# Kernel optimization log

Measured on AMD Instinct MI355X. Metric: run time of the kernel, lower is better.

The kernel has to match this reference:

```python
import jax, jax.numpy as jnp
import numpy as np

B, T, D_MODEL, N_HEAD = 2, 2048, 1024, 16
HEAD_DIM = D_MODEL // N_HEAD
CHUNK, POLY = 16, 1
SCALE = HEAD_DIM ** -0.5


def alpert_basis(L):
    # poly_order=1: constant + linear Legendre-like columns, L2-normalized per column
    t = jnp.linspace(-1.0, 1.0, L)
    W = jnp.stack([jnp.ones_like(t), t], axis=1)  # [L, 2]
    return W / jnp.linalg.norm(W, axis=0, keepdims=True)


def setup_inputs() -> dict:
    key = jax.random.key(0)
    ks = jax.random.split(key, 10)
    d = D_MODEL
    nrm = lambda k, shape, s=0.02: (jax.random.normal(k, shape, jnp.float32) * s)
    return {
        'x': jax.random.normal(ks[0], (B, T, d), jnp.float32),
        'Wq': nrm(ks[1], (d, d)),
        'Wk': nrm(ks[2], (d, d)),
        'Wv': nrm(ks[3], (d, d)),
        'Wo': nrm(ks[4], (d, d)),
        'gate_w': nrm(ks[5], (d, d)),
        'gate_b': jnp.zeros((d,), jnp.float32),
        'A': nrm(ks[6], (N_HEAD, HEAD_DIM, HEAD_DIM)),
        'jump_scale': jnp.ones((1,), jnp.float32),
        'jump_bias': jnp.zeros((1,), jnp.float32),
        'sink_scalar': nrm(ks[7], (1, N_HEAD, 1, 1)),
        'v_null': nrm(ks[8], (1, N_HEAD, 1, HEAD_DIM)),
    }


def _forward(x, Wq, Wk, Wv, Wo, gate_w, gate_b, A, jump_scale, jump_bias, sink_scalar, v_null):
    Bx, Tx, C = x.shape
    H, Dh = N_HEAD, HEAD_DIM
    NEG = jnp.float32(-1e30)

    def lin(W):  # torch Linear: y = x @ W.T, W is [out, in]
        y = jnp.einsum('btc,dc->btd', x, W)
        return y.reshape(Bx, Tx, H, Dh).transpose(0, 2, 1, 3)  # [B,H,T,Dh]

    q_raw, k_raw, v_val = lin(Wq), lin(Wk), lin(Wv)
    g = jax.nn.sigmoid(jnp.einsum('btc,dc->btd', x, gate_w) + gate_b)
    gate = g.reshape(Bx, Tx, H, Dh).transpose(0, 2, 1, 3)

    # symmetric mean/std normalization (torch std is unbiased -> ddof=1)
    ms = 0.5 * (q_raw.mean(-1, keepdims=True) + k_raw.mean(-1, keepdims=True))
    ss = 0.5 * (jnp.std(q_raw, -1, keepdims=True, ddof=1) + jnp.std(k_raw, -1, keepdims=True, ddof=1))
    q_norm = (q_raw - ms) / (ss + 1e-6)
    k_norm = (k_raw - ms) / (ss + 1e-6)

    # RoPE (half-split variant as in source)
    inv = 1.0 / (10000.0 ** (jnp.arange(0, Dh, 2, dtype=jnp.float32) / Dh))
    fr = jnp.arange(Tx, dtype=jnp.float32)[:, None] * inv[None, :]  # [T, Dh/2]
    cos, sin = jnp.cos(fr)[None, None], jnp.sin(fr)[None, None]

    def rope(z):
        z1, z2 = z[..., 0::2], z[..., 1::2]
        return jnp.concatenate([-z2 * sin + z1 * cos, z1 * sin + z2 * cos], axis=-1)

    S = A - jnp.swapaxes(A, -1, -2)  # skew-symmetric per head
    wedge = lambda z: z + jnp.einsum('bhtd,hde->bhte', z, S)
    q_geo, k_geo = wedge(rope(q_norm)), wedge(rope(k_norm))

    W_b = alpert_basis(CHUNK)  # [L, K]
    N, K, L = Tx // CHUNK, W_b.shape[1], CHUNK
    to_chunks = lambda z: z.reshape(Bx, H, N, L, Dh).transpose(2, 0, 1, 3, 4)  # [N,B,H,L,Dh]
    qx, kx, gx = to_chunks(q_geo), to_chunks(k_geo), to_chunks(gate)

    hist0 = jnp.zeros((Bx, H, N, K, Dh), jnp.float32)
    last0 = jnp.zeros((Bx, H, 1, Dh), jnp.float32)
    idx = jnp.arange(N)

    def step(carry, xs):
        hist, last, i = carry
        q_c, k_c, g_c = xs  # [B,H,L,Dh]
        k_coef = jnp.einsum('bhld,lk->bhkd', k_c, W_b)
        sc = jnp.einsum('bhkd,bhnkd->bhn', k_coef, hist) * SCALE
        sc = jnp.where(idx < i, sc, NEG)  # mask unfilled history slots
        w = jax.nn.softmax(sc, axis=-1)
        retr = jnp.einsum('bhn,bhnkd->bhkd', w, hist)
        q_rec = jnp.einsum('bhkd,lk->bhld', retr, W_b)
        jg = jax.nn.sigmoid(sc.max(-1)[..., None, None] * jump_scale + jump_bias)  # [B,H,1,1]
        inj = jnp.where(i > 0, (1.0 - jg) * last + jg * q_rec, 0.0)
        q_out = jnp.cumsum(g_c * q_c, axis=2) + inj
        hist = hist.at[:, :, i].set(jnp.einsum('bhld,lk->bhkd', q_out, W_b))
        return (hist, q_out[:, :, -1:, :], i + 1), q_out

    _, q_outs = jax.lax.scan(step, (hist0, last0, jnp.int32(0)), (qx, kx, gx))
    Q = q_outs.transpose(1, 2, 0, 3, 4).reshape(Bx, H, Tx, Dh)

    att = jnp.einsum('bhtd,bhsd->bhts', Q, k_geo) * SCALE
    causal = jnp.tril(jnp.ones((Tx, Tx), bool))
    att = jnp.where(causal, att, NEG)
    null = jnp.broadcast_to(sink_scalar, (Bx, H, Tx, 1))
    probs = jax.nn.softmax(jnp.concatenate([att, null], axis=-1), axis=-1)
    out = jnp.einsum('bhts,bhsd->bhtd', probs[..., :Tx], v_val) + probs[..., Tx:] * v_null
    out = out.transpose(0, 2, 1, 3).reshape(Bx, Tx, C)
    return jnp.einsum('btc,dc->btd', out, Wo)


def reference(x, Wq, Wk, Wv, Wo, gate_w, gate_b, A, jump_scale, jump_bias, sink_scalar, v_null):
    return _forward(x, Wq, Wk, Wv, Wo, gate_w, gate_b, A, jump_scale, jump_bias, sink_scalar, v_null)
```

## Files before the change

kernel.cpp:

```cpp
#include <hip/hip_runtime.h>
#include <math.h>

#define NB 2
#define NT 2048
#define NH 16
#define DH 64
#define DM 1024

using bf8   = __attribute__((ext_vector_type(8))) short;
using f32x4 = __attribute__((ext_vector_type(4))) float;

static __device__ __forceinline__ ushort f2bf(float f) {
    union { float f; unsigned u; } c; c.f = f;
    unsigned u = c.u + 0x7FFFu + ((c.u >> 16) & 1u);
    return (ushort)(u >> 16);
}
static __device__ __forceinline__ float bf2f(ushort u) {
    union { unsigned u; float f; } c; c.u = ((unsigned)u) << 16;
    return c.f;
}

static __device__ __forceinline__ float wbf(int l, int k) {
    if (k == 0) return 0.25f;
    const float invn = 1.0f / sqrtf(1360.0f / 225.0f);
    return (-1.0f + (2.0f / 15.0f) * (float)l) * invn;
}

__global__ __launch_bounds__(256) void cast3_kernel(
    const float* __restrict__ x, const float* __restrict__ wv,
    const float* __restrict__ wo, ushort* __restrict__ xb, ushort* __restrict__ wb)
{
    const int id = blockIdx.x * 256 + threadIdx.x;
    const int XQ = (NB * NT * DM) / 4;
    const int WQ = (DM * DM) / 4;
    const float4* src;
    ushort* dst;
    if (id < XQ) {
        src = (const float4*)x + id;
        dst = xb + (size_t)id * 4;
    } else {
        const int r = id - XQ;
        const int wi = r / WQ, off = r % WQ;
        const float* w = (wi == 0) ? wv : wo;
        src = (const float4*)w + off;
        dst = wb + (size_t)wi * DM * DM + (size_t)off * 4;
    }
    const float4 v = *src;
    ushort4 o;
    o.x = f2bf(v.x); o.y = f2bf(v.y); o.z = f2bf(v.z); o.w = f2bf(v.w);
    *(ushort4*)dst = o;
}

__global__ __launch_bounds__(256) void gemm3m_kernel(
    const float* __restrict__ x, const float* __restrict__ Wq,
    const float* __restrict__ Wk, const float* __restrict__ gw,
    const float* __restrict__ gbias,
    float* __restrict__ oq, float* __restrict__ ok, float* __restrict__ og)
{
    __shared__ ushort Ah[128][40], Am[128][40], Al[128][40];
    __shared__ ushort Bh[64][40],  Bm[64][40],  Bl[64][40];
    const int z = blockIdx.z;
    const float* Bw = (z == 0) ? Wq : (z == 1) ? Wk : gw;
    float* C = (z == 0) ? oq : (z == 1) ? ok : og;
    const int tid = threadIdx.x;
    const int l = tid & 63, w = tid >> 6;
    const int wr = w >> 1, wc = w & 1;
    const int lr = l & 15, g = l >> 4;
    const int row0 = blockIdx.y * 128, col0 = blockIdx.x * 64;
    f32x4 acc[4][2];
    #pragma unroll
    for (int mi = 0; mi < 4; ++mi)
        #pragma unroll
        for (int ni = 0; ni < 2; ++ni) acc[mi][ni] = (f32x4){0.f, 0.f, 0.f, 0.f};
    const int sa_row = tid >> 1, sa_col = (tid & 1) * 16;
    const int sb_row = tid >> 2, sb_col = (tid & 3) * 8;
    const float* Ap = x  + (size_t)(row0 + sa_row) * DM + sa_col;
    const float* Bp = Bw + (size_t)(col0 + sb_row) * DM + sb_col;
    for (int k0 = 0; k0 < DM; k0 += 32) {
        float av[16], bv[8];
        *(float4*)&av[0]  = *(const float4*)(Ap + k0);
        *(float4*)&av[4]  = *(const float4*)(Ap + k0 + 4);
        *(float4*)&av[8]  = *(const float4*)(Ap + k0 + 8);
        *(float4*)&av[12] = *(const float4*)(Ap + k0 + 12);
        *(float4*)&bv[0]  = *(const float4*)(Bp + k0);
        *(float4*)&bv[4]  = *(const float4*)(Bp + k0 + 4);
        __syncthreads();
        #pragma unroll
        for (int c = 0; c < 16; c += 4) {
            ushort4 hh, mm, ll;
            ushort* hp = (ushort*)&hh;
            ushort* mp = (ushort*)&mm;
            ushort* lp = (ushort*)&ll;
            #pragma unroll
            for (int u = 0; u < 4; ++u) {
                const float v = av[c + u];
                const ushort hu = f2bf(v);
                const float r1 = v - bf2f(hu);
                const ushort mu = f2bf(r1);
                const ushort lu = f2bf(r1 - bf2f(mu));
                hp[u] = hu; mp[u] = mu; lp[u] = lu;
            }
            *(ushort4*)&Ah[sa_row][sa_col + c] = hh;
            *(ushort4*)&Am[sa_row][sa_col + c] = mm;
            *(ushort4*)&Al[sa_row][sa_col + c] = ll;
        }
        #pragma unroll
        for (int c = 0; c < 8; c += 4) {
            ushort4 hh, mm, ll;
            ushort* hp = (ushort*)&hh;
            ushort* mp = (ushort*)&mm;
            ushort* lp = (ushort*)&ll;
            #pragma unroll
            for (int u = 0; u < 4; ++u) {
                const float v = bv[c + u];
                const ushort hu = f2bf(v);
                const float r1 = v - bf2f(hu);
                const ushort mu = f2bf(r1);
                const ushort lu = f2bf(r1 - bf2f(mu));
                hp[u] = hu; mp[u] = mu; lp[u] = lu;
            }
            *(ushort4*)&Bh[sb_row][sb_col + c] = hh;
            *(ushort4*)&Bm[sb_row][sb_col + c] = mm;
            *(ushort4*)&Bl[sb_row][sb_col + c] = ll;
        }
        __syncthreads();
        bf8 ah[4], am[4], al[4], bh[2], bm[2], bl[2];
        #pragma unroll
        for (int mi = 0; mi < 4; ++mi) {
            ah[mi] = *(const bf8*)&Ah[wr * 64 + mi * 16 + lr][g * 8];
            am[mi] = *(const bf8*)&Am[wr * 64 + mi * 16 + lr][g * 8];
            al[mi] = *(const bf8*)&Al[wr * 64 + mi * 16 + lr][g * 8];
        }
        #pragma unroll
        for (int ni = 0; ni < 2; ++ni) {
            bh[ni] = *(const bf8*)&Bh[wc * 32 + ni * 16 + lr][g * 8];
            bm[ni] = *(const bf8*)&Bm[wc * 32 + ni * 16 + lr][g * 8];
            bl[ni] = *(const bf8*)&Bl[wc * 32 + ni * 16 + lr][g * 8];
        }
        #pragma unroll
        for (int mi = 0; mi < 4; ++mi)
            #pragma unroll
            for (int ni = 0; ni < 2; ++ni) {
                acc[mi][ni] = __builtin_amdgcn_mfma_f32_16x16x32_bf16(ah[mi], bh[ni], acc[mi][ni], 0, 0, 0);
                acc[mi][ni] = __builtin_amdgcn_mfma_f32_16x16x32_bf16(ah[mi], bm[ni], acc[mi][ni], 0, 0, 0);
                acc[mi][ni] = __builtin_amdgcn_mfma_f32_16x16x32_bf16(am[mi], bh[ni], acc[mi][ni], 0, 0, 0);
                acc[mi][ni] = __builtin_amdgcn_mfma_f32_16x16x32_bf16(am[mi], bm[ni], acc[mi][ni], 0, 0, 0);
                acc[mi][ni] = __builtin_amdgcn_mfma_f32_16x16x32_bf16(ah[mi], bl[ni], acc[mi][ni], 0, 0, 0);
                acc[mi][ni] = __builtin_amdgcn_mfma_f32_16x16x32_bf16(al[mi], bh[ni], acc[mi][ni], 0, 0, 0);
            }
    }
    #pragma unroll
    for (int mi = 0; mi < 4; ++mi) {
        const int m0 = row0 + wr * 64 + mi * 16 + g * 4;
        const int bb = m0 >> 11, t0 = m0 & 2047;
        #pragma unroll
        for (int ni = 0; ni < 2; ++ni) {
            const int n = col0 + wc * 32 + ni * 16 + lr;
            const int h = n >> 6, dh = n & 63;
            #pragma unroll
            for (int r = 0; r < 4; ++r) {
                float v = acc[mi][ni][r];
                if (z == 2) v = 1.0f / (1.0f + __expf(-(v + gbias[n])));
                C[(((size_t)(bb * NH + h)) * NT + (t0 + r)) * DH + dh] = v;
            }
        }
    }
}

__global__ __launch_bounds__(256) void gemm_bf16_kernel(
    const ushort* __restrict__ Ab, const ushort* __restrict__ Bb,
    float* __restrict__ Cp)
{
    __shared__ ushort Al[128][40];
    __shared__ ushort Bl[64][40];
    const int tid = threadIdx.x;
    const int l = tid & 63, w = tid >> 6;
    const int wr = w >> 1, wc = w & 1;
    const int lr = l & 15, g = l >> 4;
    const int row0 = blockIdx.y * 128, col0 = blockIdx.x * 64;
    f32x4 acc[4][2];
    #pragma unroll
    for (int mi = 0; mi < 4; ++mi)
        #pragma unroll
        for (int ni = 0; ni < 2; ++ni) acc[mi][ni] = (f32x4){0.f, 0.f, 0.f, 0.f};
    const int sa_row = tid >> 1, sa_half = (tid & 1) * 16;
    const int sb_row = tid >> 2, sb_q = (tid & 3) * 8;
    const ushort* Ap = Ab + (size_t)(row0 + sa_row) * DM + sa_half;
    const ushort* Bp = Bb + (size_t)(col0 + sb_row) * DM + sb_q;
    for (int k0 = 0; k0 < DM; k0 += 32) {
        const uint4 a0 = *(const uint4*)(Ap + k0);
        const uint4 a1 = *(const uint4*)(Ap + k0 + 8);
        const uint4 b0 = *(const uint4*)(Bp + k0);
        __syncthreads();
        *(uint4*)&Al[sa_row][sa_half]     = a0;
        *(uint4*)&Al[sa_row][sa_half + 8] = a1;
        *(uint4*)&Bl[sb_row][sb_q]        = b0;
        __syncthreads();
        bf8 a[4], b[2];
        #pragma unroll
        for (int mi = 0; mi < 4; ++mi) a[mi] = *(const bf8*)&Al[wr * 64 + mi * 16 + lr][g * 8];
        #pragma unroll
        for (int ni = 0; ni < 2; ++ni) b[ni] = *(const bf8*)&Bl[wc * 32 + ni * 16 + lr][g * 8];
        #pragma unroll
        for (int mi = 0; mi < 4; ++mi)
            #pragma unroll
            for (int ni = 0; ni < 2; ++ni)
                acc[mi][ni] = __builtin_amdgcn_mfma_f32_16x16x32_bf16(a[mi], b[ni], acc[mi][ni], 0, 0, 0);
    }
    #pragma unroll
    for (int mi = 0; mi < 4; ++mi) {
        const int m0 = row0 + wr * 64 + mi * 16 + g * 4;
        #pragma unroll
        for (int ni = 0; ni < 2; ++ni) {
            const int n = col0 + wc * 32 + ni * 16 + lr;
            #pragma unroll
            for (int r = 0; r < 4; ++r)
                Cp[(size_t)(m0 + r) * DM + n] = acc[mi][ni][r];
        }
    }
}

__global__ __launch_bounds__(256) void nrw_kernel(
    const float* __restrict__ qraw, const float* __restrict__ kraw,
    const float* __restrict__ Amat, float* __restrict__ gateq,
    ushort* __restrict__ kgb,
    float* __restrict__ kcoefA, float* __restrict__ R0A,
    float* __restrict__ R1A, float* __restrict__ r15A)
{
    __shared__ float S[64][64];
    __shared__ float zq[4][64];
    __shared__ float zk[4][64];
    const int bh = blockIdx.x;
    const int h = bh & (NH - 1);
    const int tid = threadIdx.x;
    const int g = tid >> 6, lane = tid & 63;
    for (int idx = tid; idx < 4096; idx += 256) {
        const int d = idx >> 6, e = idx & 63;
        S[d][e] = Amat[(size_t)h * 4096 + d * 64 + e] - Amat[(size_t)h * 4096 + e * 64 + d];
    }
    __syncthreads();
    const int j = lane & 31;
    const float invf = powf(10000.0f, -(float)(2 * j) * (1.0f / 64.0f));
    const int t0 = blockIdx.y * 64 + g * 16;
    float kc0 = 0.f, kc1 = 0.f, run = 0.f, Ra0 = 0.f, Ra1 = 0.f;
    for (int r = 0; r < 16; ++r) {
        const int t = t0 + r;
        const size_t base = ((size_t)bh * NT + t) * DH;
        const float qv = qraw[base + lane];
        const float kv = kraw[base + lane];
        float sq = qv, sk = kv, qq = qv * qv, kk2 = kv * kv;
        #pragma unroll
        for (int off = 32; off; off >>= 1) {
            sq += __shfl_xor(sq, off);
            sk += __shfl_xor(sk, off);
            qq += __shfl_xor(qq, off);
            kk2 += __shfl_xor(kk2, off);
        }
        const float mq = sq * (1.0f / 64.0f), mk = sk * (1.0f / 64.0f);
        const float vq = (qq - 64.0f * mq * mq) * (1.0f / 63.0f);
        const float vk = (kk2 - 64.0f * mk * mk) * (1.0f / 63.0f);
        const float ms = 0.5f * (mq + mk);
        const float ss = 0.5f * (sqrtf(fmaxf(vq, 0.0f)) + sqrtf(fmaxf(vk, 0.0f)));
        const float rinv = 1.0f / (ss + 1e-6f);
        const float qn = (qv - ms) * rinv;
        const float kn = (kv - ms) * rinv;
        const float q1 = __shfl(qn, 2 * j), q2 = __shfl(qn, 2 * j + 1);
        const float k1 = __shfl(kn, 2 * j), k2 = __shfl(kn, 2 * j + 1);
        float sn, cs;
        sincosf((float)t * invf, &sn, &cs);
        const float rq = (lane < 32) ? (q1 * cs - q2 * sn) : (q1 * sn + q2 * cs);
        const float rk = (lane < 32) ? (k1 * cs - k2 * sn) : (k1 * sn + k2 * cs);
        zq[g][lane] = rq;
        zk[g][lane] = rk;
        float aq = 0.0f, ak = 0.0f;
        #pragma unroll 8
        for (int d = 0; d < 64; ++d) {
            const float sde = S[d][lane];
            aq = fmaf(zq[g][d], sde, aq);
            ak = fmaf(zk[g][d], sde, ak);
        }
        const float qgv = rq + aq;
        const float kgv = rk + ak;
        const float gv = gateq[base + lane];
        const float qgpv = gv * qgv;
        gateq[base + lane] = qgpv;
        kgb[base + lane] = f2bf(kgv);
        kc0 = fmaf(kgv, 0.25f, kc0);
        kc1 = fmaf(kgv, wbf(r, 1), kc1);
        run += qgpv;
        Ra0 = fmaf(run, 0.25f, Ra0);
        Ra1 = fmaf(run, wbf(r, 1), Ra1);
    }
    const int unit = bh * 128 + blockIdx.y * 4 + g;
    kcoefA[(size_t)unit * 128 + lane] = kc0;
    kcoefA[(size_t)unit * 128 + 64 + lane] = kc1;
    R0A[(size_t)unit * 64 + lane] = Ra0;
    R1A[(size_t)unit * 64 + lane] = Ra1;
    r15A[(size_t)unit * 64 + lane] = run;
}

__global__ __launch_bounds__(256) void scan_vgemm_kernel(
    const float* __restrict__ kcoefA, const float* __restrict__ R0A,
    const float* __restrict__ R1A, const float* __restrict__ r15A,
    const float* __restrict__ jscale, const float* __restrict__ jbias,
    float* __restrict__ r0O, float* __restrict__ r1O,
    float* __restrict__ lpO, float* __restrict__ jgO,
    const ushort* __restrict__ xb, const ushort* __restrict__ Wb,
    ushort* __restrict__ Vt)
{
    __shared__ char smem[100864];
    if (blockIdx.x >= 32) {
        const int gi = blockIdx.x - 32;
        const int col0 = (gi & 15) * 64;
        const int row0 = (gi >> 4) * 128;
        ushort (*Al)[40] = (ushort(*)[40])smem;
        ushort (*Bl)[40] = (ushort(*)[40])(smem + 10240);
        const int tid = threadIdx.x;
        const int l = tid & 63, w = tid >> 6;
        const int wr = w >> 1, wc = w & 1;
        const int lr = l & 15, g = l >> 4;
        f32x4 acc[4][2];
        #pragma unroll
        for (int mi = 0; mi < 4; ++mi)
            #pragma unroll
            for (int ni = 0; ni < 2; ++ni) acc[mi][ni] = (f32x4){0.f, 0.f, 0.f, 0.f};
        const int sa_row = tid >> 1, sa_half = (tid & 1) * 16;
        const int sb_row = tid >> 2, sb_q = (tid & 3) * 8;
        const ushort* Ap = xb + (size_t)(row0 + sa_row) * DM + sa_half;
        const ushort* Bp = Wb + (size_t)(col0 + sb_row) * DM + sb_q;
        for (int k0 = 0; k0 < DM; k0 += 32) {
            const uint4 a0 = *(const uint4*)(Ap + k0);
            const uint4 a1 = *(const uint4*)(Ap + k0 + 8);
            const uint4 b0 = *(const uint4*)(Bp + k0);
            __syncthreads();
            *(uint4*)&Al[sa_row][sa_half]     = a0;
            *(uint4*)&Al[sa_row][sa_half + 8] = a1;
            *(uint4*)&Bl[sb_row][sb_q]        = b0;
            __syncthreads();
            bf8 a[4], b[2];
            #pragma unroll
            for (int mi = 0; mi < 4; ++mi) a[mi] = *(const bf8*)&Al[wr * 64 + mi * 16 + lr][g * 8];
            #pragma unroll
            for (int ni = 0; ni < 2; ++ni) b[ni] = *(const bf8*)&Bl[wc * 32 + ni * 16 + lr][g * 8];
            #pragma unroll
            for (int mi = 0; mi < 4; ++mi)
                #pragma unroll
                for (int ni = 0; ni < 2; ++ni)
                    acc[mi][ni] = __builtin_amdgcn_mfma_f32_16x16x32_bf16(a[mi], b[ni], acc[mi][ni], 0, 0, 0);
        }
        #pragma unroll
        for (int mi = 0; mi < 4; ++mi) {
            const int m0 = row0 + wr * 64 + mi * 16 + g * 4;
            const int bb = m0 >> 11, t0 = m0 & 2047;
            #pragma unroll
            for (int ni = 0; ni < 2; ++ni) {
                const int n = col0 + wc * 32 + ni * 16 + lr;
                const int h = n >> 6, dh = n & 63;
                ushort4 pk;
                pk.x = f2bf(acc[mi][ni][0]); pk.y = f2bf(acc[mi][ni][1]);
                pk.z = f2bf(acc[mi][ni][2]); pk.w = f2bf(acc[mi][ni][3]);
                *(ushort4*)(Vt + (((size_t)(bb * NH + h)) * DH + dh) * NT + t0) = pk;
            }
        }
        return;
    }
    if (threadIdx.x >= 64) return;
    float* HA  = (float*)smem;
    float* KcL = (float*)(smem + 65536);
    float* EL  = (float*)(smem + 73728);
    float* ET  = (float*)(smem + 82176);
    float* VP  = (float*)(smem + 92416);
    float* mxold = (float*)(smem + 100608);
    float* psold = (float*)(smem + 100672);
    float* pbuf  = (float*)(smem + 100736);
    float* qbuf    = (float*)(smem + 73728);
    float* candBuf = (float*)(smem + 74752);
    const int bh = blockIdx.x;
    const int l = threadIdx.x;
    #pragma unroll
    for (int c = 0; c < 64; ++c)
        *(f32x4*)&HA[c * 256 + l * 4] = (f32x4){0.f, 0.f, 0.f, 0.f};
    const float js = jscale[0], jb = jbias[0];
    const float* kcp  = kcoefA + (size_t)bh * 128 * 128;
    const float* R0p  = R0A  + (size_t)bh * 128 * 64;
    const float* R1p  = R1A  + (size_t)bh * 128 * 64;
    const float* r15p = r15A + (size_t)bh * 128 * 64;
    float* r0o = r0O + (size_t)bh * 128 * 64;
    float* r1o = r1O + (size_t)bh * 128 * 64;
    float* lpo = lpO + (size_t)bh * 128 * 64;
    float* jgo = jgO + (size_t)bh * 128;
    float last = 0.0f;
    const float wb15_1 = wbf(15, 1);
    const int iiq = l >> 2, sq = l & 3;
    const int ch = l >> 2;

    for (int j = 0; j < 8; ++j) {
        const int P = 16 * j;
        #pragma unroll
        for (int t = 0; t < 8; ++t)
            *(f32x4*)&KcL[t * 256 + l * 4] = *(const f32x4*)&kcp[j * 2048 + t * 256 + l * 4];
        float R0b[16], R1b[16], r15b[16];
        #pragma unroll
        for (int t = 0; t < 16; ++t) {
            R0b[t]  = R0p[(P + t) * 64 + l];
            R1b[t]  = R1p[(P + t) * 64 + l];
            r15b[t] = r15p[(P + t) * 64 + l];
        }
        {
            float sA[16], sB[16];
            #pragma unroll
            for (int ii = 0; ii < 16; ++ii) { sA[ii] = 0.f; sB[ii] = 0.f; }
            const int swA = l & 31;
            for (int c = 0; c < 32; ++c) {
                const int cs = ((c ^ swA) << 2);
                const f32x4 hA = *(const f32x4*)&HA[l * 128 + cs];
                const f32x4 hB = *(const f32x4*)&HA[(64 + l) * 128 + cs];
                #pragma unroll
                for (int ii = 0; ii < 16; ++ii) {
                    const f32x4 kc = *(const f32x4*)&KcL[ii * 128 + (c << 2)];
                    sA[ii] = fmaf(hA[0], kc[0], sA[ii]); sA[ii] = fmaf(hA[1], kc[1], sA[ii]);
                    sA[ii] = fmaf(hA[2], kc[2], sA[ii]); sA[ii] = fmaf(hA[3], kc[3], sA[ii]);
                    sB[ii] = fmaf(hB[0], kc[0], sB[ii]); sB[ii] = fmaf(hB[1], kc[1], sB[ii]);
                    sB[ii] = fmaf(hB[2], kc[2], sB[ii]); sB[ii] = fmaf(hB[3], kc[3], sB[ii]);
                }
            }
            #pragma unroll
            for (int ii = 0; ii < 16; ++ii) {
                if (l < P)      EL[ii * 132 + l]      = sA[ii] * 0.125f;
                if (64 + l < P) EL[ii * 132 + 64 + l] = sB[ii] * 0.125f;
            }
        }
        {
            float m = -1e30f;
            for (int n = sq; n < P; n += 4) m = fmaxf(m, EL[iiq * 132 + n]);
            m = fmaxf(m, __shfl_xor(m, 1));
            m = fmaxf(m, __shfl_xor(m, 2));
            if (sq == 0) mxold[iiq] = m;
        }
        {
            const float mo = (P > 0) ? mxold[iiq] : -1e30f;
            float ps = 0.f;
            for (int n = sq; n < P; n += 4) {
                const float e = __expf(EL[iiq * 132 + n] - mo);
                ET[n * 20 + iiq] = e;
                ps += e;
            }
            ps += __shfl_xor(ps, 1);
            ps += __shfl_xor(ps, 2);
            if (sq == 0) psold[iiq] = ps;
        }
        {
            float vp0[16], vp1[16];
            #pragma unroll
            for (int ii = 0; ii < 16; ++ii) { vp0[ii] = 0.f; vp1[ii] = 0.f; }
            for (int n = 0; n < P; ++n) {
                const int sw = n & 31;
                const float h0 = HA[n * 128 + ((ch ^ sw) << 2) + (l & 3)];
                const float h1 = HA[n * 128 + (((16 + ch) ^ sw) << 2) + (l & 3)];
                const f32x4 e0 = *(const f32x4*)&ET[n * 20];
                const f32x4 e1 = *(const f32x4*)&ET[n * 20 + 4];
                const f32x4 e2 = *(const f32x4*)&ET[n * 20 + 8];
                const f32x4 e3 = *(const f32x4*)&ET[n * 20 + 12];
                #pragma unroll
                for (int u = 0; u < 4; ++u) {
                    vp0[u]      = fmaf(e0[u], h0, vp0[u]);      vp1[u]      = fmaf(e0[u], h1, vp1[u]);
                    vp0[4 + u]  = fmaf(e1[u], h0, vp0[4 + u]);  vp1[4 + u]  = fmaf(e1[u], h1, vp1[4 + u]);
                    vp0[8 + u]  = fmaf(e2[u], h0, vp0[8 + u]);  vp1[8 + u]  = fmaf(e2[u], h1, vp1[8 + u]);
                    vp0[12 + u] = fmaf(e3[u], h0, vp0[12 + u]); vp1[12 + u] = fmaf(e3[u], h1, vp1[12 + u]);
                }
            }
            #pragma unroll
            for (int ii = 0; ii < 16; ++ii) {
                VP[ii * 128 + l]      = vp0[ii];
                VP[ii * 128 + 64 + l] = vp1[ii];
            }
        }
        const int n_ = l >> 2, q = l & 3;
        const int qb = l & ~3;
        #pragma unroll
        for (int iL = 0; iL < 16; ++iL) {
            const int i = P + iL;
            const int nrow = P + n_;
            const int nsw = nrow & 31;
            float scp = 0.f;
            #pragma unroll
            for (int c = 0; c < 8; ++c) {
                const f32x4 h  = *(const f32x4*)&HA[nrow * 128 + ((((q << 3) + c) ^ nsw) << 2)];
                const f32x4 kc = *(const f32x4*)&KcL[iL * 128 + (q << 5) + (c << 2)];
                scp = fmaf(h[0], kc[0], scp); scp = fmaf(h[1], kc[1], scp);
                scp = fmaf(h[2], kc[2], scp); scp = fmaf(h[3], kc[3], scp);
            }
            qbuf[l] = scp;
            const float scn = (qbuf[qb] + qbuf[qb + 1]) + (qbuf[qb + 2] + qbuf[qb + 3]);
            const float cand = (n_ < iL) ? scn * 0.125f : -1e30f;
            if (q == 0) candBuf[n_] = cand;
            float m8[8];
            #pragma unroll
            for (int u = 0; u < 8; ++u) m8[u] = fmaxf(candBuf[2 * u], candBuf[2 * u + 1]);
            float m4a = fmaxf(m8[0], m8[1]), m4b = fmaxf(m8[2], m8[3]);
            float m4c = fmaxf(m8[4], m8[5]), m4d = fmaxf(m8[6], m8[7]);
            const float mxn = fmaxf(fmaxf(m4a, m4b), fmaxf(m4c, m4d));
            const float mo = mxold[iL];
            const float mx = fmaxf(mxn, mo);
            const float p = (n_ < iL) ? __expf(cand - mx) : 0.f;
            if (q == 0) pbuf[n_] = p;
            float s8[8];
            #pragma unroll
            for (int u = 0; u < 8; ++u) s8[u] = pbuf[2 * u] + pbuf[2 * u + 1];
            float s4a = s8[0] + s8[1], s4b = s8[2] + s8[3];
            float s4c = s8[4] + s8[5], s4d = s8[6] + s8[7];
            const float psn = (s4a + s4b) + (s4c + s4d);
            float r0 = 0.f, r1 = 0.f;
            if (i > 0) {
                const float so = __expf(mo - mx);
                float racc0 = VP[iL * 128 + l] * so;
                float racc1 = VP[iL * 128 + 64 + l] * so;
                #pragma unroll
                for (int n2 = 0; n2 < iL; ++n2) {
                    const float pn = pbuf[n2];
                    const int nr = P + n2;
                    const int sw2 = nr & 31;
                    racc0 = fmaf(pn, HA[nr * 128 + ((ch ^ sw2) << 2) + (l & 3)], racc0);
                    racc1 = fmaf(pn, HA[nr * 128 + (((16 + ch) ^ sw2) << 2) + (l & 3)], racc1);
                }
                const float ps = fmaf(psold[iL], so, psn);
                const float rden = 1.0f / ps;
                r0 = racc0 * rden;
                r1 = racc1 * rden;
            }
            const float jg = 1.0f / (1.0f + __expf(-fmaf(mx, js, jb)));
            const float lastp = last;
            const float h0n = R0b[iL] + fmaf(jg, r0, 4.0f * (1.0f - jg) * lastp);
            const float h1n = fmaf(jg, r1, R1b[iL]);
            const float qrec15 = fmaf(r0, 0.25f, r1 * wb15_1);
            last = r15b[iL] + fmaf(jg, qrec15, (1.0f - jg) * lastp);
            r0o[i * 64 + l] = r0;
            r1o[i * 64 + l] = r1;
            lpo[i * 64 + l] = lastp;
            if (l == 0) jgo[i] = jg;
            const int swi = i & 31;
            HA[i * 128 + ((ch ^ swi) << 2) + (l & 3)] = h0n;
            HA[i * 128 + (((16 + ch) ^ swi) << 2) + (l & 3)] = h1n;
        }
    }
}

__global__ __launch_bounds__(256) void scan_post_kernel(
    const float* __restrict__ qgp, const float* __restrict__ r0O,
    const float* __restrict__ r1O, const float* __restrict__ lpO,
    const float* __restrict__ jgO, float* __restrict__ Qout)
{
    const int unit = blockIdx.x * 4 + (threadIdx.x >> 6);
    const int d = threadIdx.x & 63;
    const int bh = unit >> 7, i = unit & 127;
    const size_t ub = (size_t)unit * 64 + d;
    const float r0 = r0O[ub], r1 = r1O[ub], lp = lpO[ub];
    const float jg = jgO[unit];
    const size_t cbase = ((size_t)bh * NT + i * 16) * DH + d;
    float run = 0.0f;
    #pragma unroll
    for (int ll = 0; ll < 16; ++ll) {
        run += qgp[cbase + ll * 64];
        const float qrec = fmaf(r0, 0.25f, r1 * wbf(ll, 1));
        const float inj = (i > 0) ? fmaf(jg, qrec, (1.0f - jg) * lp) : 0.0f;
        Qout[cbase + ll * 64] = run + inj;
    }
}

__global__ __launch_bounds__(256) void attn_mfma_kernel(
    const float* __restrict__ Qf, const ushort* __restrict__ Kb,
    const ushort* __restrict__ Vtb, const float* __restrict__ sink,
    const float* __restrict__ vnull, ushort* __restrict__ Ob)
{
    __shared__ ushort Kl0[64][40], Kl1[64][40];
    __shared__ ushort Vl0[64][40], Vl1[64][40];
    __shared__ ushort Pl[4][2][16][40];
    const int bh = blockIdx.y;
    const int h = bh & (NH - 1);
    const int b = bh >> 4;
    const int qt = gridDim.x - 1 - blockIdx.x;
    const int q0 = qt * 64;
    const int tid = threadIdx.x;
    const int w = tid >> 6, l = tid & 63;
    const int lr = l & 15, g = l >> 4;
    bf8 qf[2];
    {
        const float* qp = Qf + (((size_t)bh * NT) + q0 + 16 * w + lr) * DH + g * 8;
        #pragma unroll
        for (int ks = 0; ks < 2; ++ks) {
            const float4 f0 = *(const float4*)(qp + 32 * ks);
            const float4 f1 = *(const float4*)(qp + 32 * ks + 4);
            bf8 q;
            q[0] = (short)f2bf(f0.x); q[1] = (short)f2bf(f0.y);
            q[2] = (short)f2bf(f0.z); q[3] = (short)f2bf(f0.w);
            q[4] = (short)f2bf(f1.x); q[5] = (short)f2bf(f1.y);
            q[6] = (short)f2bf(f1.z); q[7] = (short)f2bf(f1.w);
            qf[ks] = q;
        }
    }
    f32x4 oacc[4];
    #pragma unroll
    for (int nf2 = 0; nf2 < 4; ++nf2) oacc[nf2] = (f32x4){0.f, 0.f, 0.f, 0.f};
    float mrow[4], lrowp[4];
    #pragma unroll
    for (int r = 0; r < 4; ++r) { mrow[r] = -1e30f; lrowp[r] = 0.0f; }
    const int ntiles = qt + 1;
    const ushort* Kg = Kb + (size_t)bh * NT * DH;
    const ushort* Vg = Vtb + (size_t)bh * DH * NT;
    const int srow = tid >> 2;
    const int sc16 = (tid & 3) * 16;
    for (int it = 0; it < ntiles; ++it) {
        const int kv0 = it * 64;
        __syncthreads();
        {
            const ushort* kp = Kg + (size_t)(kv0 + srow) * DH + sc16;
            const ushort* vp = Vg + (size_t)srow * NT + kv0 + sc16;
            ushort* kd = (sc16 < 32) ? &Kl0[srow][sc16] : &Kl1[srow][sc16 - 32];
            ushort* vd = (sc16 < 32) ? &Vl0[srow][sc16] : &Vl1[srow][sc16 - 32];
            *(uint4*)kd       = *(const uint4*)kp;
            *(uint4*)(kd + 8) = *(const uint4*)(kp + 8);
            *(uint4*)vd       = *(const uint4*)vp;
            *(uint4*)(vd + 8) = *(const uint4*)(vp + 8);
        }
        __syncthreads();
        f32x4 s[4];
        #pragma unroll
        for (int nf = 0; nf < 4; ++nf) {
            s[nf] = (f32x4){0.f, 0.f, 0.f, 0.f};
            const bf8 kf0 = *(const bf8*)&Kl0[nf * 16 + lr][g * 8];
            const bf8 kf1 = *(const bf8*)&Kl1[nf * 16 + lr][g * 8];
            s[nf] = __builtin_amdgcn_mfma_f32_16x16x32_bf16(qf[0], kf0, s[nf], 0, 0, 0);
            s[nf] = __builtin_amdgcn_mfma_f32_16x16x32_bf16(qf[1], kf1, s[nf], 0, 0, 0);
        }
        #pragma unroll
        for (int r = 0; r < 4; ++r) {
            const int row = q0 + 16 * w + g * 4 + r;
            float sv[4];
            float tmax = -1e30f;
            #pragma unroll
            for (int nf = 0; nf < 4; ++nf) {
                const int col = kv0 + nf * 16 + lr;
                sv[nf] = (col <= row) ? s[nf][r] * 0.125f : -1e30f;
                tmax = fmaxf(tmax, sv[nf]);
            }
            tmax = fmaxf(tmax, __shfl_xor(tmax, 1));
            tmax = fmaxf(tmax, __shfl_xor(tmax, 2));
            tmax = fmaxf(tmax, __shfl_xor(tmax, 4));
            tmax = fmaxf(tmax, __shfl_xor(tmax, 8));
            const float mnew = fmaxf(mrow[r], tmax);
            const float csc = __expf(mrow[r] - mnew);
            float plocal = 0.f;
            #pragma unroll
            for (int nf = 0; nf < 4; ++nf) {
                const float p = __expf(sv[nf] - mnew);
                plocal += p;
                Pl[w][nf >> 1][g * 4 + r][(nf & 1) * 16 + lr] = f2bf(p);
            }
            lrowp[r] = lrowp[r] * csc + plocal;
            mrow[r] = mnew;
            #pragma unroll
            for (int nf2 = 0; nf2 < 4; ++nf2) oacc[nf2][r] *= csc;
        }
        const bf8 pa0 = *(const bf8*)&Pl[w][0][lr][g * 8];
        const bf8 pa1 = *(const bf8*)&Pl[w][1][lr][g * 8];
        #pragma unroll
        for (int nf2 = 0; nf2 < 4; ++nf2) {
            const bf8 vb0 = *(const bf8*)&Vl0[nf2 * 16 + lr][g * 8];
            const bf8 vb1 = *(const bf8*)&Vl1[nf2 * 16 + lr][g * 8];
            oacc[nf2] = __builtin_amdgcn_mfma_f32_16x16x32_bf16(pa0, vb0, oacc[nf2], 0, 0, 0);
            oacc[nf2] = __builtin_amdgcn_mfma_f32_16x16x32_bf16(pa1, vb1, oacc[nf2], 0, 0, 0);
        }
    }
    float lrow[4];
    #pragma unroll
    for (int r = 0; r < 4; ++r) {
        float ps = lrowp[r];
        ps += __shfl_xor(ps, 1);
        ps += __shfl_xor(ps, 2);
        ps += __shfl_xor(ps, 4);
        ps += __shfl_xor(ps, 8);
        lrow[r] = ps;
    }
    const float s0 = sink[h];
    float c0v[4], pnv[4], rden[4];
    #pragma unroll
    for (int r = 0; r < 4; ++r) {
        const float mf = fmaxf(mrow[r], s0);
        c0v[r] = __expf(mrow[r] - mf);
        pnv[r] = __expf(s0 - mf);
        rden[r] = 1.0f / fmaf(lrow[r], c0v[r], pnv[r]);
    }
    #pragma unroll
    for (int nf2 = 0; nf2 < 4; ++nf2) {
        const float vn = vnull[h * DH + nf2 * 16 + lr];
        #pragma unroll
        for (int r = 0; r < 4; ++r) {
            const float out = fmaf(pnv[r], vn, oacc[nf2][r] * c0v[r]) * rden[r];
            const int trow = q0 + 16 * w + g * 4 + r;
            Ob[(((size_t)b * NT) + trow) * DM + h * DH + nf2 * 16 + lr] = f2bf(out);
        }
    }
}

extern "C" void kernel_launch(void* const* d_in, const int* in_sizes, int n_in,
                              void* d_out, int out_size, void* d_ws, size_t ws_size,
                              hipStream_t stream) {
    const float* x     = (const float*)d_in[0];
    const float* Wq    = (const float*)d_in[1];
    const float* Wk    = (const float*)d_in[2];
    const float* Wv    = (const float*)d_in[3];
    const float* Wo    = (const float*)d_in[4];
    const float* gw    = (const float*)d_in[5];
    const float* gbias = (const float*)d_in[6];
    const float* Amat  = (const float*)d_in[7];
    const float* js    = (const float*)d_in[8];
    const float* jb    = (const float*)d_in[9];
    const float* sink  = (const float*)d_in[10];
    const float* vnull = (const float*)d_in[11];
    char* ws = (char*)d_ws;
    const size_t MB = 1024 * 1024;
    float*  q_raw  = (float*)(ws + 0);
    float*  k_raw  = (float*)(ws + 16 * MB);
    float*  gate   = (float*)(ws + 32 * MB);
    ushort* kgb    = (ushort*)(ws + 64 * MB);
    ushort* xb     = (ushort*)(ws + 72 * MB);
    ushort* Wb     = (ushort*)(ws + 80 * MB);
    float*  kcoefA = (float*)(ws + 84 * MB);
    float*  R0A    = (float*)(ws + 86 * MB);
    float*  R1A    = (float*)(ws + 87 * MB);
    float*  r15A   = (float*)(ws + 88 * MB);
    float*  r0O    = (float*)(ws + 89 * MB);
    float*  r1O    = (float*)(ws + 90 * MB);
    float*  lpO    = (float*)(ws + 91 * MB);
    float*  jgO    = (float*)(ws + 92 * MB);
    ushort* Vt     = (ushort*)k_raw;
    ushort* attob  = (ushort*)(ws + 24 * MB);

    cast3_kernel<<<6144, 256, 0, stream>>>(x, Wv, Wo, xb, Wb);
    gemm3m_kernel<<<dim3(DM / 64, (NB * NT) / 128, 3), 256, 0, stream>>>(
        x, Wq, Wk, gw, gbias, q_raw, k_raw, gate);
    nrw_kernel<<<dim3(NB * NH, NT / 64), 256, 0, stream>>>(
        q_raw, k_raw, Amat, gate, kgb, kcoefA, R0A, R1A, r15A);
    scan_vgemm_kernel<<<32 + 512, 256, 0, stream>>>(
        kcoefA, R0A, R1A, r15A, js, jb, r0O, r1O, lpO, jgO, xb, Wb, Vt);
    scan_post_kernel<<<1024, 256, 0, stream>>>(gate, r0O, r1O, lpO, jgO, q_raw);
    attn_mfma_kernel<<<dim3(NT / 64, NB * NH), 256, 0, stream>>>(q_raw, kgb, Vt, sink, vnull, attob);
    gemm_bf16_kernel<<<dim3(DM / 64, (NB * NT) / 128), 256, 0, stream>>>(
        attob, Wb + DM * DM, (float*)d_out);
}
```

Before: 664.0 us.

## Spread per-chunk scan score and value-projection work across four wavefronts

The sequential scan block previously ran on a single 64-thread wavefront and left the other three waves of the 256-thread block idle. Now all four waves zero the history buffer, load the coefficient chunk, and split the 16 query rows of the history-score and value-projection passes, four rows each. Only the inherently sequential softmax-recurrence inner loop stays on wave 0. This shortens the chunk-parallel phases at the cost of several block-wide barriers per chunk.

```diff
diff --git a/kernel.cpp b/kernel.cpp
--- a/kernel.cpp
+++ b/kernel.cpp
@@ -364,7 +364,6 @@
         }
         return;
     }
-    if (threadIdx.x >= 64) return;
     float* HA  = (float*)smem;
     float* KcL = (float*)(smem + 65536);
     float* EL  = (float*)(smem + 73728);
@@ -376,10 +375,11 @@
     float* qbuf    = (float*)(smem + 73728);
     float* candBuf = (float*)(smem + 74752);
     const int bh = blockIdx.x;
-    const int l = threadIdx.x;
-    #pragma unroll
-    for (int c = 0; c < 64; ++c)
-        *(f32x4*)&HA[c * 256 + l * 4] = (f32x4){0.f, 0.f, 0.f, 0.f};
+    const int tid = threadIdx.x;
+    const int l = tid & 63, w = tid >> 6;
+    #pragma unroll
+    for (int c = 0; c < 16; ++c)
+        *(f32x4*)&HA[c * 1024 + tid * 4] = (f32x4){0.f, 0.f, 0.f, 0.f};
     const float js = jscale[0], jb = jbias[0];
     const float* kcp  = kcoefA + (size_t)bh * 128 * 128;
     const float* R0p  = R0A  + (size_t)bh * 128 * 64;
@@ -396,49 +396,49 @@
 
     for (int j = 0; j < 8; ++j) {
         const int P = 16 * j;
-        #pragma unroll
-        for (int t = 0; t < 8; ++t)
-            *(f32x4*)&KcL[t * 256 + l * 4] = *(const f32x4*)&kcp[j * 2048 + t * 256 + l * 4];
+        *(f32x4*)&KcL[tid * 8]     = *(const f32x4*)&kcp[j * 2048 + tid * 8];
+        *(f32x4*)&KcL[tid * 8 + 4] = *(const f32x4*)&kcp[j * 2048 + tid * 8 + 4];
         float R0b[16], R1b[16], r15b[16];
-        #pragma unroll
-        for (int t = 0; t < 16; ++t) {
-            R0b[t]  = R0p[(P + t) * 64 + l];
-            R1b[t]  = R1p[(P + t) * 64 + l];
-            r15b[t] = r15p[(P + t) * 64 + l];
-        }
+        if (w == 0) {
+            #pragma unroll
+            for (int t = 0; t < 16; ++t) {
+                R0b[t]  = R0p[(P + t) * 64 + l];
+                R1b[t]  = R1p[(P + t) * 64 + l];
+                r15b[t] = r15p[(P + t) * 64 + l];
+            }
+        }
+        __syncthreads();
         {
-            float sA[16], sB[16];
-            #pragma unroll
-            for (int ii = 0; ii < 16; ++ii) { sA[ii] = 0.f; sB[ii] = 0.f; }
+            float sA[4] = {0.f, 0.f, 0.f, 0.f};
+            float sB[4] = {0.f, 0.f, 0.f, 0.f};
             const int swA = l & 31;
             for (int c = 0; c < 32; ++c) {
                 const int cs = ((c ^ swA) << 2);
                 const f32x4 hA = *(const f32x4*)&HA[l * 128 + cs];
                 const f32x4 hB = *(const f32x4*)&HA[(64 + l) * 128 + cs];
                 #pragma unroll
-                for (int ii = 0; ii < 16; ++ii) {
-                    const f32x4 kc = *(const f32x4*)&KcL[ii * 128 + (c << 2)];
-                    sA[ii] = fmaf(hA[0], kc[0], sA[ii]); sA[ii] = fmaf(hA[1], kc[1], sA[ii]);
-                    sA[ii] = fmaf(hA[2], kc[2], sA[ii]); sA[ii] = fmaf(hA[3], kc[3], sA[ii]);
-                    sB[ii] = fmaf(hB[0], kc[0], sB[ii]); sB[ii] = fmaf(hB[1], kc[1], sB[ii]);
-                    sB[ii] = fmaf(hB[2], kc[2], sB[ii]); sB[ii] = fmaf(hB[3], kc[3], sB[ii]);
+                for (int t = 0; t < 4; ++t) {
+                    const f32x4 kc = *(const f32x4*)&KcL[(4 * w + t) * 128 + (c << 2)];
+                    sA[t] = fmaf(hA[0], kc[0], sA[t]); sA[t] = fmaf(hA[1], kc[1], sA[t]);
+                    sA[t] = fmaf(hA[2], kc[2], sA[t]); sA[t] = fmaf(hA[3], kc[3], sA[t]);
+                    sB[t] = fmaf(hB[0], kc[0], sB[t]); sB[t] = fmaf(hB[1], kc[1], sB[t]);
+                    sB[t] = fmaf(hB[2], kc[2], sB[t]); sB[t] = fmaf(hB[3], kc[3], sB[t]);
                 }
             }
             #pragma unroll
-            for (int ii = 0; ii < 16; ++ii) {
-                if (l < P)      EL[ii * 132 + l]      = sA[ii] * 0.125f;
-                if (64 + l < P) EL[ii * 132 + 64 + l] = sB[ii] * 0.125f;
-            }
-        }
-        {
+            for (int t = 0; t < 4; ++t) {
+                if (l < P)      EL[(4 * w + t) * 132 + l]      = sA[t] * 0.125f;
+                if (64 + l < P) EL[(4 * w + t) * 132 + 64 + l] = sB[t] * 0.125f;
+            }
+        }
+        __syncthreads();
+        if (w == 0) {
             float m = -1e30f;
             for (int n = sq; n < P; n += 4) m = fmaxf(m, EL[iiq * 132 + n]);
             m = fmaxf(m, __shfl_xor(m, 1));
             m = fmaxf(m, __shfl_xor(m, 2));
             if (sq == 0) mxold[iiq] = m;
-        }
-        {
-            const float mo = (P > 0) ? mxold[iiq] : -1e30f;
+            const float mo = (P > 0) ? m : -1e30f;
             float ps = 0.f;
             for (int n = sq; n < P; n += 4) {
                 const float e = __expf(EL[iiq * 132 + n] - mo);
@@ -449,99 +449,98 @@
             ps += __shfl_xor(ps, 2);
             if (sq == 0) psold[iiq] = ps;
         }
+        __syncthreads();
         {
-            float vp0[16], vp1[16];
-            #pragma unroll
-            for (int ii = 0; ii < 16; ++ii) { vp0[ii] = 0.f; vp1[ii] = 0.f; }
+            float vp0[4] = {0.f, 0.f, 0.f, 0.f};
+            float vp1[4] = {0.f, 0.f, 0.f, 0.f};
             for (int n = 0; n < P; ++n) {
                 const int sw = n & 31;
                 const float h0 = HA[n * 128 + ((ch ^ sw) << 2) + (l & 3)];
                 const float h1 = HA[n * 128 + (((16 + ch) ^ sw) << 2) + (l & 3)];
-                const f32x4 e0 = *(const f32x4*)&ET[n * 20];
-                const f32x4 e1 = *(const f32x4*)&ET[n * 20 + 4];
-                const f32x4 e2 = *(const f32x4*)&ET[n * 20 + 8];
-                const f32x4 e3 = *(const f32x4*)&ET[n * 20 + 12];
+                const f32x4 e = *(const f32x4*)&ET[n * 20 + 4 * w];
                 #pragma unroll
                 for (int u = 0; u < 4; ++u) {
-                    vp0[u]      = fmaf(e0[u], h0, vp0[u]);      vp1[u]      = fmaf(e0[u], h1, vp1[u]);
-                    vp0[4 + u]  = fmaf(e1[u], h0, vp0[4 + u]);  vp1[4 + u]  = fmaf(e1[u], h1, vp1[4 + u]);
-                    vp0[8 + u]  = fmaf(e2[u], h0, vp0[8 + u]);  vp1[8 + u]  = fmaf(e2[u], h1, vp1[8 + u]);
-                    vp0[12 + u] = fmaf(e3[u], h0, vp0[12 + u]); vp1[12 + u] = fmaf(e3[u], h1, vp1[12 + u]);
+                    vp0[u] = fmaf(e[u], h0, vp0[u]);
+                    vp1[u] = fmaf(e[u], h1, vp1[u]);
                 }
             }
             #pragma unroll
-            for (int ii = 0; ii < 16; ++ii) {
-                VP[ii * 128 + l]      = vp0[ii];
-                VP[ii * 128 + 64 + l] = vp1[ii];
-            }
-        }
-        const int n_ = l >> 2, q = l & 3;
-        const int qb = l & ~3;
-        #pragma unroll
-        for (int iL = 0; iL < 16; ++iL) {
-            const int i = P + iL;
-            const int nrow = P + n_;
-            const int nsw = nrow & 31;
-            float scp = 0.f;
-            #pragma unroll
-            for (int c = 0; c < 8; ++c) {
-                const f32x4 h  = *(const f32x4*)&HA[nrow * 128 + ((((q << 3) + c) ^ nsw) << 2)];
-                const f32x4 kc = *(const f32x4*)&KcL[iL * 128 + (q << 5) + (c << 2)];
-                scp = fmaf(h[0], kc[0], scp); scp = fmaf(h[1], kc[1], scp);
-                scp = fmaf(h[2], kc[2], scp); scp = fmaf(h[3], kc[3], scp);
-            }
-            qbuf[l] = scp;
-            const float scn = (qbuf[qb] + qbuf[qb + 1]) + (qbuf[qb + 2] + qbuf[qb + 3]);
-            const float cand = (n_ < iL) ? scn * 0.125f : -1e30f;
-            if (q == 0) candBuf[n_] = cand;
-            float m8[8];
-            #pragma unroll
-            for (int u = 0; u < 8; ++u) m8[u] = fmaxf(candBuf[2 * u], candBuf[2 * u + 1]);
-            float m4a = fmaxf(m8[0], m8[1]), m4b = fmaxf(m8[2], m8[3]);
-            float m4c = fmaxf(m8[4], m8[5]), m4d = fmaxf(m8[6], m8[7]);
-            const float mxn = fmaxf(fmaxf(m4a, m4b), fmaxf(m4c, m4d));
-            const float mo = mxold[iL];
-            const float mx = fmaxf(mxn, mo);
-            const float p = (n_ < iL) ? __expf(cand - mx) : 0.f;
-            if (q == 0) pbuf[n_] = p;
-            float s8[8];
-            #pragma unroll
-            for (int u = 0; u < 8; ++u) s8[u] = pbuf[2 * u] + pbuf[2 * u + 1];
-            float s4a = s8[0] + s8[1], s4b = s8[2] + s8[3];
-            float s4c = s8[4] + s8[5], s4d = s8[6] + s8[7];
-            const float psn = (s4a + s4b) + (s4c + s4d);
-            float r0 = 0.f, r1 = 0.f;
-            if (i > 0) {
-                const float so = __expf(mo - mx);
-                float racc0 = VP[iL * 128 + l] * so;
-                float racc1 = VP[iL * 128 + 64 + l] * so;
+            for (int u = 0; u < 4; ++u) {
+                VP[(4 * w + u) * 128 + l]      = vp0[u];
+                VP[(4 * w + u) * 128 + 64 + l] = vp1[u];
+            }
+        }
+        __syncthreads();
+        if (w == 0) {
+            const int n_ = l >> 2, q = l & 3;
+            const int qb = l & ~3;
+            #pragma unroll
+            for (int iL = 0; iL < 16; ++iL) {
+                const int i = P + iL;
+                const int nrow = P + n_;
+                const int nsw = nrow & 31;
+                float scp = 0.f;
                 #pragma unroll
-                for (int n2 = 0; n2 < iL; ++n2) {
-                    const float pn = pbuf[n2];
-                    const int nr = P + n2;
-                    const int sw2 = nr & 31;
-                    racc0 = fmaf(pn, HA[nr * 128 + ((ch ^ sw2) << 2) + (l & 3)], racc0);
-                    racc1 = fmaf(pn, HA[nr * 128 + (((16 + ch) ^ sw2) << 2) + (l & 3)], racc1);
+                for (int c = 0; c < 8; ++c) {
+                    const f32x4 h  = *(const f32x4*)&HA[nrow * 128 + ((((q << 3) + c) ^ nsw) << 2)];
+                    const f32x4 kc = *(const f32x4*)&KcL[iL * 128 + (q << 5) + (c << 2)];
+                    scp = fmaf(h[0], kc[0], scp); scp = fmaf(h[1], kc[1], scp);
+                    scp = fmaf(h[2], kc[2], scp); scp = fmaf(h[3], kc[3], scp);
                 }
-                const float ps = fmaf(psold[iL], so, psn);
-                const float rden = 1.0f / ps;
-                r0 = racc0 * rden;
-                r1 = racc1 * rden;
-            }
-            const float jg = 1.0f / (1.0f + __expf(-fmaf(mx, js, jb)));
-            const float lastp = last;
-            const float h0n = R0b[iL] + fmaf(jg, r0, 4.0f * (1.0f - jg) * lastp);
-            const float h1n = fmaf(jg, r1, R1b[iL]);
-            const float qrec15 = fmaf(r0, 0.25f, r1 * wb15_1);
-            last = r15b[iL] + fmaf(jg, qrec15, (1.0f - jg) * lastp);
-            r0o[i * 64 + l] = r0;
-            r1o[i * 64 + l] = r1;
-            lpo[i * 64 + l] = lastp;
-            if (l == 0) jgo[i] = jg;
-            const int swi = i & 31;
-            HA[i * 128 + ((ch ^ swi) << 2) + (l & 3)] = h0n;
-            HA[i * 128 + (((16 + ch) ^ swi) << 2) + (l & 3)] = h1n;
-        }
+                qbuf[l] = scp;
+                const float scn = (qbuf[qb] + qbuf[qb + 1]) + (qbuf[qb + 2] + qbuf[qb + 3]);
+                const float cand = (n_ < iL) ? scn * 0.125f : -1e30f;
+                if (q == 0) candBuf[n_] = cand;
+                float m8[8];
+                #pragma unroll
+                for (int u = 0; u < 8; ++u) m8[u] = fmaxf(candBuf[2 * u], candBuf[2 * u + 1]);
+                float m4a = fmaxf(m8[0], m8[1]), m4b = fmaxf(m8[2], m8[3]);
+                float m4c = fmaxf(m8[4], m8[5]), m4d = fmaxf(m8[6], m8[7]);
+                const float mxn = fmaxf(fmaxf(m4a, m4b), fmaxf(m4c, m4d));
+                const float mo = mxold[iL];
+                const float mx = fmaxf(mxn, mo);
+                const float p = (n_ < iL) ? __expf(cand - mx) : 0.f;
+                if (q == 0) pbuf[n_] = p;
+                float s8[8];
+                #pragma unroll
+                for (int u = 0; u < 8; ++u) s8[u] = pbuf[2 * u] + pbuf[2 * u + 1];
+                float s4a = s8[0] + s8[1], s4b = s8[2] + s8[3];
+                float s4c = s8[4] + s8[5], s4d = s8[6] + s8[7];
+                const float psn = (s4a + s4b) + (s4c + s4d);
+                float r0 = 0.f, r1 = 0.f;
+                if (i > 0) {
+                    const float so = __expf(mo - mx);
+                    float racc0 = VP[iL * 128 + l] * so;
+                    float racc1 = VP[iL * 128 + 64 + l] * so;
+                    #pragma unroll
+                    for (int n2 = 0; n2 < iL; ++n2) {
+                        const float pn = pbuf[n2];
+                        const int nr = P + n2;
+                        const int sw2 = nr & 31;
+                        racc0 = fmaf(pn, HA[nr * 128 + ((ch ^ sw2) << 2) + (l & 3)], racc0);
+                        racc1 = fmaf(pn, HA[nr * 128 + (((16 + ch) ^ sw2) << 2) + (l & 3)], racc1);
+                    }
+                    const float ps = fmaf(psold[iL], so, psn);
+                    const float rden = 1.0f / ps;
+                    r0 = racc0 * rden;
+                    r1 = racc1 * rden;
+                }
+                const float jg = 1.0f / (1.0f + __expf(-fmaf(mx, js, jb)));
+                const float lastp = last;
+                const float h0n = R0b[iL] + fmaf(jg, r0, 4.0f * (1.0f - jg) * lastp);
+                const float h1n = fmaf(jg, r1, R1b[iL]);
+                const float qrec15 = fmaf(r0, 0.25f, r1 * wb15_1);
+                last = r15b[iL] + fmaf(jg, qrec15, (1.0f - jg) * lastp);
+                r0o[i * 64 + l] = r0;
+                r1o[i * 64 + l] = r1;
+                lpo[i * 64 + l] = lastp;
+                if (l == 0) jgo[i] = jg;
+                const int swi = i & 31;
+                HA[i * 128 + ((ch ^ swi) << 2) + (l & 3)] = h0n;
+                HA[i * 128 + (((16 + ch) ^ swi) << 2) + (l & 3)] = h1n;
+            }
+        }
+        __syncthreads();
     }
 }
 
```

Result: slower. 815.1 us (+22.7%).
